# Performance work log

Hardware: AMD Instinct MI355X
Metric: run time of the kernel (lower is better)

The kernel has to match this reference:

```python
import jax, jax.numpy as jnp
import numpy as np

B, S, D_IN, RANK, D_OUT = 8, 1024, 1280, 64, 1280
DOWN_SIZE = RANK * D_IN      # 81920
UP_SIZE = D_OUT * RANK       # 81920


def setup_inputs() -> dict:
    key = jax.random.key(0)
    k1, k2 = jax.random.split(key)
    x = jax.random.normal(k1, (B, S, D_IN), dtype=jnp.float32)
    # per-image embedding that encodes the dynamic LoRA weights
    embed = jax.random.normal(k2, (B, DOWN_SIZE + UP_SIZE), dtype=jnp.float32) * 0.02
    return {"x": x, "embed": embed}


def reference(x, embed):
    # down_forward: per-sample weight = embed[:, :down_size].view(down_shape)=[rank, d_in]
    # original does x_chunk @ W.T per sample; batched as a single grouped GEMM
    w_down = embed[:, :DOWN_SIZE].reshape(B, RANK, D_IN)   # [B, r, d_in]
    h = jnp.einsum('bsd,brd->bsr', x, w_down)              # x @ W_down.T, batched
    # up_forward: per-sample weight = embed[:, -up_size:].view(up_shape)=[d_out, rank]
    w_up = embed[:, -UP_SIZE:].reshape(B, D_OUT, RANK)     # [B, d_out, r]
    out = jnp.einsum('bsr,bor->bso', h, w_up)              # h @ W_up.T, batched
    return out
```

## Files before the change

### kernel.cpp

```cpp
#include <hip/hip_runtime.h>

#define NB   8
#define S_   1024
#define DIN  1280
#define RANK 64
#define DOUT 1280
#define DOWN (RANK * DIN)
#define EMB  (DOWN + DOUT * RANK)
#define XSTRIDE 1288

typedef __bf16 bf16x8 __attribute__((ext_vector_type(8)));
typedef __bf16 bf16x4 __attribute__((ext_vector_type(4)));
typedef float  f32x4  __attribute__((ext_vector_type(4)));

__global__ __launch_bounds__(256) void cvt_embed(const float* __restrict__ src,
                                                 __bf16* __restrict__ dst, int n8) {
    const int i = blockIdx.x * 256 + threadIdx.x;
    if (i < n8) {
        const float4* s = reinterpret_cast<const float4*>(src) + (size_t)i * 2;
        float4 f0 = s[0], f1 = s[1];
        bf16x8 v;
        v[0]=(__bf16)f0.x; v[1]=(__bf16)f0.y; v[2]=(__bf16)f0.z; v[3]=(__bf16)f0.w;
        v[4]=(__bf16)f1.x; v[5]=(__bf16)f1.y; v[6]=(__bf16)f1.z; v[7]=(__bf16)f1.w;
        *reinterpret_cast<bf16x8*>(dst + (size_t)i * 8) = v;
    }
}

__global__ __launch_bounds__(512, 2) void lora_main(const float* __restrict__ x,
                                                    const __bf16* __restrict__ ew,
                                                    float* __restrict__ out) {
    __shared__ __bf16 xls[16 * XSTRIDE];
    __shared__ float  pbuf[4][16][20];
    __shared__ __bf16 hld[16][80];

    const int b    = blockIdx.x & 7;
    const int s0   = (blockIdx.x >> 3) * 16;
    const int t    = threadIdx.x;
    const int w    = t >> 6;
    const int l    = t & 63;
    const int quad = l >> 4;
    const int lc   = l & 15;
    const int dq   = quad * 8;

    {
        const int row = t >> 5;
        const int c   = t & 31;
        const float4* src = reinterpret_cast<const float4*>(x + (size_t)(b * S_ + s0 + row) * DIN);
        __bf16* drow = xls + row * XSTRIDE;
#pragma unroll
        for (int j = 0; j < 10; ++j) {
            float4 f = src[c + 32 * j];
            bf16x4 v;
            v[0]=(__bf16)f.x; v[1]=(__bf16)f.y; v[2]=(__bf16)f.z; v[3]=(__bf16)f.w;
            *reinterpret_cast<bf16x4*>(drow + c * 4 + 128 * j) = v;
        }
    }
    __syncthreads();

    const int nt = w & 3;
    const int kh = w >> 2;
    const __bf16* wdrow  = ew + (size_t)b * EMB + (size_t)(nt * 16 + lc) * DIN + kh * 640;
    const __bf16* xlsrow = xls + lc * XSTRIDE + kh * 640;

    f32x4 acc = {0,0,0,0};
#pragma unroll 5
    for (int ks = 0; ks < 20; ++ks) {
        const int k = ks * 32 + dq;
        bf16x8 af = *reinterpret_cast<const bf16x8*>(xlsrow + k);
        bf16x8 bf = *reinterpret_cast<const bf16x8*>(wdrow + k);
        acc = __builtin_amdgcn_mfma_f32_16x16x32_bf16(af, bf, acc, 0, 0, 0);
    }

    if (kh == 1) {
#pragma unroll
        for (int i = 0; i < 4; ++i) pbuf[nt][quad * 4 + i][lc] = acc[i];
    }
    __syncthreads();
    if (kh == 0) {
#pragma unroll
        for (int i = 0; i < 4; ++i) {
            float v = acc[i] + pbuf[nt][quad * 4 + i][lc];
            hld[quad * 4 + i][nt * 16 + lc] = (__bf16)v;
        }
    }
    __syncthreads();

    bf16x8 ha0 = *reinterpret_cast<const bf16x8*>(&hld[lc][dq]);
    bf16x8 ha1 = *reinterpret_cast<const bf16x8*>(&hld[lc][32 + dq]);
    const __bf16* wu    = ew + (size_t)b * EMB + DOWN;
    float*        obase = out + (size_t)(b * S_ + s0 + quad * 4) * DOUT;

#pragma unroll 2
    for (int tt = 0; tt < 10; ++tt) {
        const int n = w + 8 * tt;
        const int o = n * 16 + lc;
        bf16x8 b0 = *reinterpret_cast<const bf16x8*>(wu + (size_t)o * RANK + dq);
        bf16x8 b1 = *reinterpret_cast<const bf16x8*>(wu + (size_t)o * RANK + 32 + dq);
        f32x4 c = {0,0,0,0};
        c = __builtin_amdgcn_mfma_f32_16x16x32_bf16(ha0, b0, c, 0, 0, 0);
        c = __builtin_amdgcn_mfma_f32_16x16x32_bf16(ha1, b1, c, 0, 0, 0);
#pragma unroll
        for (int i = 0; i < 4; ++i)
            obase[(size_t)i * DOUT + o] = c[i];
    }
}

extern "C" void kernel_launch(void* const* d_in, const int* in_sizes, int n_in,
                              void* d_out, int out_size, void* d_ws, size_t ws_size,
                              hipStream_t stream) {
    const float* x     = (const float*)d_in[0];
    const float* embed = (const float*)d_in[1];
    float*       out   = (float*)d_out;
    __bf16*      ew    = (__bf16*)d_ws;
    (void)in_sizes; (void)n_in; (void)out_size; (void)ws_size;

    cvt_embed<<<dim3(640), dim3(256), 0, stream>>>(embed, ew, NB * EMB / 8);
    lora_main<<<dim3(512), dim3(512), 0, stream>>>(x, ew, out);
}
```

Before: 109.3 us.

## Split fused LoRA kernel into separate down and up kernels with split-K partials

Splits the fused LoRA kernel into two. The down projection runs as 1024 smaller blocks, each handling half of the K dimension and writing fp32 partial h values to workspace. The up projection kernel sums the two partials, converts them to bf16 and does the second GEMM. This aims to raise parallelism and occupancy and shrink the shared-memory footprint, at the cost of an extra launch and a global round trip for the partial h values.

```diff
diff --git a/kernel.cpp b/kernel.cpp
--- a/kernel.cpp
+++ b/kernel.cpp
@@ -7,11 +7,20 @@
 #define DOUT 1280
 #define DOWN (RANK * DIN)
 #define EMB  (DOWN + DOUT * RANK)
-#define XSTRIDE 1288
+#define XSTR 648
 
 typedef __bf16 bf16x8 __attribute__((ext_vector_type(8)));
 typedef __bf16 bf16x4 __attribute__((ext_vector_type(4)));
 typedef float  f32x4  __attribute__((ext_vector_type(4)));
+
+#define PH_OFF (NB * EMB)
+
+__device__ __forceinline__ bf16x8 cvt8(float4 a, float4 b) {
+    bf16x8 r;
+    r[0] = (__bf16)a.x; r[1] = (__bf16)a.y; r[2] = (__bf16)a.z; r[3] = (__bf16)a.w;
+    r[4] = (__bf16)b.x; r[5] = (__bf16)b.y; r[6] = (__bf16)b.z; r[7] = (__bf16)b.w;
+    return r;
+}
 
 __global__ __launch_bounds__(256) void cvt_embed(const float* __restrict__ src,
                                                  __bf16* __restrict__ dst, int n8) {
@@ -19,22 +28,19 @@
     if (i < n8) {
         const float4* s = reinterpret_cast<const float4*>(src) + (size_t)i * 2;
         float4 f0 = s[0], f1 = s[1];
-        bf16x8 v;
-        v[0]=(__bf16)f0.x; v[1]=(__bf16)f0.y; v[2]=(__bf16)f0.z; v[3]=(__bf16)f0.w;
-        v[4]=(__bf16)f1.x; v[5]=(__bf16)f1.y; v[6]=(__bf16)f1.z; v[7]=(__bf16)f1.w;
-        *reinterpret_cast<bf16x8*>(dst + (size_t)i * 8) = v;
+        *reinterpret_cast<bf16x8*>(dst + (size_t)i * 8) = cvt8(f0, f1);
     }
 }
 
-__global__ __launch_bounds__(512, 2) void lora_main(const float* __restrict__ x,
+__global__ __launch_bounds__(256, 4) void lora_down(const float* __restrict__ x,
                                                     const __bf16* __restrict__ ew,
-                                                    float* __restrict__ out) {
-    __shared__ __bf16 xls[16 * XSTRIDE];
-    __shared__ float  pbuf[4][16][20];
-    __shared__ __bf16 hld[16][80];
+                                                    float* __restrict__ ph) {
+    __shared__ __bf16 xls[16 * XSTR];
 
-    const int b    = blockIdx.x & 7;
-    const int s0   = (blockIdx.x >> 3) * 16;
+    const int bid  = blockIdx.x;
+    const int b    = bid & 7;
+    const int st   = (bid >> 3) & 63;
+    const int kh   = bid >> 9;
     const int t    = threadIdx.x;
     const int w    = t >> 6;
     const int l    = t & 63;
@@ -43,62 +49,83 @@
     const int dq   = quad * 8;
 
     {
-        const int row = t >> 5;
-        const int c   = t & 31;
-        const float4* src = reinterpret_cast<const float4*>(x + (size_t)(b * S_ + s0 + row) * DIN);
-        __bf16* drow = xls + row * XSTRIDE;
+        const int row = t >> 4;
+        const int c   = t & 15;
+        const float4* src = reinterpret_cast<const float4*>(
+            x + (size_t)(b * S_ + st * 16 + row) * DIN + kh * 640);
+        __bf16* drow = xls + row * XSTR;
 #pragma unroll
         for (int j = 0; j < 10; ++j) {
-            float4 f = src[c + 32 * j];
+            float4 f = src[c + 16 * j];
             bf16x4 v;
             v[0]=(__bf16)f.x; v[1]=(__bf16)f.y; v[2]=(__bf16)f.z; v[3]=(__bf16)f.w;
-            *reinterpret_cast<bf16x4*>(drow + c * 4 + 128 * j) = v;
+            *reinterpret_cast<bf16x4*>(drow + (c + 16 * j) * 4) = v;
         }
     }
     __syncthreads();
 
-    const int nt = w & 3;
-    const int kh = w >> 2;
-    const __bf16* wdrow  = ew + (size_t)b * EMB + (size_t)(nt * 16 + lc) * DIN + kh * 640;
-    const __bf16* xlsrow = xls + lc * XSTRIDE + kh * 640;
+    const __bf16* wdrow = ew + (size_t)b * EMB + (size_t)(w * 16 + lc) * DIN + kh * 640;
+    const __bf16* xrow  = xls + lc * XSTR;
 
     f32x4 acc = {0,0,0,0};
-#pragma unroll 5
+#pragma unroll 10
     for (int ks = 0; ks < 20; ++ks) {
         const int k = ks * 32 + dq;
-        bf16x8 af = *reinterpret_cast<const bf16x8*>(xlsrow + k);
+        bf16x8 af = *reinterpret_cast<const bf16x8*>(xrow + k);
         bf16x8 bf = *reinterpret_cast<const bf16x8*>(wdrow + k);
         acc = __builtin_amdgcn_mfma_f32_16x16x32_bf16(af, bf, acc, 0, 0, 0);
     }
 
-    if (kh == 1) {
+    float* pdst = ph + ((((size_t)kh * NB + b) * 64 + st) * 16) * 64;
 #pragma unroll
-        for (int i = 0; i < 4; ++i) pbuf[nt][quad * 4 + i][lc] = acc[i];
+    for (int i = 0; i < 4; ++i)
+        pdst[(size_t)(quad * 4 + i) * 64 + w * 16 + lc] = acc[i];
+}
+
+__global__ __launch_bounds__(512, 4) void lora_up(const float* __restrict__ ph,
+                                                  const __bf16* __restrict__ ew,
+                                                  float* __restrict__ out) {
+    const int bid  = blockIdx.x;
+    const int b    = bid & 7;
+    const int st   = bid >> 3;
+    const int w    = threadIdx.x >> 6;
+    const int l    = threadIdx.x & 63;
+    const int quad = l >> 4;
+    const int lc   = l & 15;
+    const int dq   = quad * 8;
+
+    const float* p0 = ph + (((size_t)b * 64 + st) * 16 + lc) * 64;
+    const float* p1 = p0 + (size_t)NB * 64 * 16 * 64;
+    f32x4 a00 = *reinterpret_cast<const f32x4*>(p0 + dq);
+    f32x4 a01 = *reinterpret_cast<const f32x4*>(p0 + dq + 4);
+    f32x4 a10 = *reinterpret_cast<const f32x4*>(p0 + 32 + dq);
+    f32x4 a11 = *reinterpret_cast<const f32x4*>(p0 + 32 + dq + 4);
+    f32x4 b00 = *reinterpret_cast<const f32x4*>(p1 + dq);
+    f32x4 b01 = *reinterpret_cast<const f32x4*>(p1 + dq + 4);
+    f32x4 b10 = *reinterpret_cast<const f32x4*>(p1 + 32 + dq);
+    f32x4 b11 = *reinterpret_cast<const f32x4*>(p1 + 32 + dq + 4);
+    f32x4 s0 = a00 + b00, s1 = a01 + b01, s2 = a10 + b10, s3 = a11 + b11;
+    bf16x8 ha0, ha1;
+#pragma unroll
+    for (int j = 0; j < 4; ++j) {
+        ha0[j]     = (__bf16)s0[j];
+        ha0[4 + j] = (__bf16)s1[j];
+        ha1[j]     = (__bf16)s2[j];
+        ha1[4 + j] = (__bf16)s3[j];
     }
-    __syncthreads();
-    if (kh == 0) {
-#pragma unroll
-        for (int i = 0; i < 4; ++i) {
-            float v = acc[i] + pbuf[nt][quad * 4 + i][lc];
-            hld[quad * 4 + i][nt * 16 + lc] = (__bf16)v;
-        }
-    }
-    __syncthreads();
 
-    bf16x8 ha0 = *reinterpret_cast<const bf16x8*>(&hld[lc][dq]);
-    bf16x8 ha1 = *reinterpret_cast<const bf16x8*>(&hld[lc][32 + dq]);
     const __bf16* wu    = ew + (size_t)b * EMB + DOWN;
-    float*        obase = out + (size_t)(b * S_ + s0 + quad * 4) * DOUT;
+    float*        obase = out + (size_t)(b * S_ + st * 16 + quad * 4) * DOUT;
 
 #pragma unroll 2
     for (int tt = 0; tt < 10; ++tt) {
         const int n = w + 8 * tt;
         const int o = n * 16 + lc;
-        bf16x8 b0 = *reinterpret_cast<const bf16x8*>(wu + (size_t)o * RANK + dq);
-        bf16x8 b1 = *reinterpret_cast<const bf16x8*>(wu + (size_t)o * RANK + 32 + dq);
+        bf16x8 w0 = *reinterpret_cast<const bf16x8*>(wu + (size_t)o * RANK + dq);
+        bf16x8 w1 = *reinterpret_cast<const bf16x8*>(wu + (size_t)o * RANK + 32 + dq);
         f32x4 c = {0,0,0,0};
-        c = __builtin_amdgcn_mfma_f32_16x16x32_bf16(ha0, b0, c, 0, 0, 0);
-        c = __builtin_amdgcn_mfma_f32_16x16x32_bf16(ha1, b1, c, 0, 0, 0);
+        c = __builtin_amdgcn_mfma_f32_16x16x32_bf16(ha0, w0, c, 0, 0, 0);
+        c = __builtin_amdgcn_mfma_f32_16x16x32_bf16(ha1, w1, c, 0, 0, 0);
 #pragma unroll
         for (int i = 0; i < 4; ++i)
             obase[(size_t)i * DOUT + o] = c[i];
@@ -112,8 +139,10 @@
     const float* embed = (const float*)d_in[1];
     float*       out   = (float*)d_out;
     __bf16*      ew    = (__bf16*)d_ws;
+    float*       ph    = (float*)((char*)d_ws + (size_t)NB * EMB * 2);
     (void)in_sizes; (void)n_in; (void)out_size; (void)ws_size;
 
     cvt_embed<<<dim3(640), dim3(256), 0, stream>>>(embed, ew, NB * EMB / 8);
-    lora_main<<<dim3(512), dim3(512), 0, stream>>>(x, ew, out);
+    lora_down<<<dim3(1024), dim3(256), 0, stream>>>(x, ew, ph);
+    lora_up<<<dim3(512), dim3(512), 0, stream>>>(ph, ew, out);
 }
```

Result: slower. 115.1 us (+5.2%).

## Stage up-projection output through LDS for coalesced float4 stores and prefetch weights

Applied to the files above, without the earlier changes.

The up-projection results are now written into a shared-memory buffer that reuses the x staging area. They are then stored to global memory as contiguous float4 rows in 256-column chunks, replacing scattered 4-byte stores. The first eight down-projection weight fragments are loaded before the x staging, and the next chunk's up-projection weights are fetched while the current chunk is written out. The launch-bounds occupancy hint rises to 4 blocks per CU; this adds more barriers per block and may increase register pressure.

```diff
diff --git a/kernel.cpp b/kernel.cpp
--- a/kernel.cpp
+++ b/kernel.cpp
@@ -7,11 +7,19 @@
 #define DOUT 1280
 #define DOWN (RANK * DIN)
 #define EMB  (DOWN + DOUT * RANK)
-#define XSTRIDE 1288
+#define XSTR 1288
+#define OSTR 268
 
 typedef __bf16 bf16x8 __attribute__((ext_vector_type(8)));
 typedef __bf16 bf16x4 __attribute__((ext_vector_type(4)));
 typedef float  f32x4  __attribute__((ext_vector_type(4)));
+
+__device__ __forceinline__ bf16x8 cvt8(float4 a, float4 b) {
+    bf16x8 r;
+    r[0] = (__bf16)a.x; r[1] = (__bf16)a.y; r[2] = (__bf16)a.z; r[3] = (__bf16)a.w;
+    r[4] = (__bf16)b.x; r[5] = (__bf16)b.y; r[6] = (__bf16)b.z; r[7] = (__bf16)b.w;
+    return r;
+}
 
 __global__ __launch_bounds__(256) void cvt_embed(const float* __restrict__ src,
                                                  __bf16* __restrict__ dst, int n8) {
@@ -19,17 +27,17 @@
     if (i < n8) {
         const float4* s = reinterpret_cast<const float4*>(src) + (size_t)i * 2;
         float4 f0 = s[0], f1 = s[1];
-        bf16x8 v;
-        v[0]=(__bf16)f0.x; v[1]=(__bf16)f0.y; v[2]=(__bf16)f0.z; v[3]=(__bf16)f0.w;
-        v[4]=(__bf16)f1.x; v[5]=(__bf16)f1.y; v[6]=(__bf16)f1.z; v[7]=(__bf16)f1.w;
-        *reinterpret_cast<bf16x8*>(dst + (size_t)i * 8) = v;
+        *reinterpret_cast<bf16x8*>(dst + (size_t)i * 8) = cvt8(f0, f1);
     }
 }
 
-__global__ __launch_bounds__(512, 2) void lora_main(const float* __restrict__ x,
+__global__ __launch_bounds__(512, 4) void lora_main(const float* __restrict__ x,
                                                     const __bf16* __restrict__ ew,
                                                     float* __restrict__ out) {
-    __shared__ __bf16 xls[16 * XSTRIDE];
+    __shared__ union {
+        __bf16 xls[16 * XSTR];
+        float  obuf[16 * OSTR];
+    } u;
     __shared__ float  pbuf[4][16][20];
     __shared__ __bf16 hld[16][80];
 
@@ -42,31 +50,51 @@
     const int lc   = l & 15;
     const int dq   = quad * 8;
 
+    const int nt = w & 3;
+    const int kh = w >> 2;
+    const __bf16* wdrow = ew + (size_t)b * EMB + (size_t)(nt * 16 + lc) * DIN + kh * 640;
+
+    bf16x8 pf0 = *reinterpret_cast<const bf16x8*>(wdrow + 0 * 32 + dq);
+    bf16x8 pf1 = *reinterpret_cast<const bf16x8*>(wdrow + 1 * 32 + dq);
+    bf16x8 pf2 = *reinterpret_cast<const bf16x8*>(wdrow + 2 * 32 + dq);
+    bf16x8 pf3 = *reinterpret_cast<const bf16x8*>(wdrow + 3 * 32 + dq);
+    bf16x8 pf4 = *reinterpret_cast<const bf16x8*>(wdrow + 4 * 32 + dq);
+    bf16x8 pf5 = *reinterpret_cast<const bf16x8*>(wdrow + 5 * 32 + dq);
+    bf16x8 pf6 = *reinterpret_cast<const bf16x8*>(wdrow + 6 * 32 + dq);
+    bf16x8 pf7 = *reinterpret_cast<const bf16x8*>(wdrow + 7 * 32 + dq);
+
     {
         const int row = t >> 5;
         const int c   = t & 31;
         const float4* src = reinterpret_cast<const float4*>(x + (size_t)(b * S_ + s0 + row) * DIN);
-        __bf16* drow = xls + row * XSTRIDE;
+        __bf16* drow = u.xls + row * XSTR;
 #pragma unroll
         for (int j = 0; j < 10; ++j) {
             float4 f = src[c + 32 * j];
             bf16x4 v;
             v[0]=(__bf16)f.x; v[1]=(__bf16)f.y; v[2]=(__bf16)f.z; v[3]=(__bf16)f.w;
-            *reinterpret_cast<bf16x4*>(drow + c * 4 + 128 * j) = v;
+            *reinterpret_cast<bf16x4*>(drow + (c + 32 * j) * 4) = v;
         }
     }
     __syncthreads();
 
-    const int nt = w & 3;
-    const int kh = w >> 2;
-    const __bf16* wdrow  = ew + (size_t)b * EMB + (size_t)(nt * 16 + lc) * DIN + kh * 640;
-    const __bf16* xlsrow = xls + lc * XSTRIDE + kh * 640;
-
+    const __bf16* xrow = u.xls + lc * XSTR + kh * 640;
     f32x4 acc = {0,0,0,0};
-#pragma unroll 5
-    for (int ks = 0; ks < 20; ++ks) {
+    {
+        bf16x8 af;
+        af = *reinterpret_cast<const bf16x8*>(xrow + 0*32 + dq); acc = __builtin_amdgcn_mfma_f32_16x16x32_bf16(af, pf0, acc, 0,0,0);
+        af = *reinterpret_cast<const bf16x8*>(xrow + 1*32 + dq); acc = __builtin_amdgcn_mfma_f32_16x16x32_bf16(af, pf1, acc, 0,0,0);
+        af = *reinterpret_cast<const bf16x8*>(xrow + 2*32 + dq); acc = __builtin_amdgcn_mfma_f32_16x16x32_bf16(af, pf2, acc, 0,0,0);
+        af = *reinterpret_cast<const bf16x8*>(xrow + 3*32 + dq); acc = __builtin_amdgcn_mfma_f32_16x16x32_bf16(af, pf3, acc, 0,0,0);
+        af = *reinterpret_cast<const bf16x8*>(xrow + 4*32 + dq); acc = __builtin_amdgcn_mfma_f32_16x16x32_bf16(af, pf4, acc, 0,0,0);
+        af = *reinterpret_cast<const bf16x8*>(xrow + 5*32 + dq); acc = __builtin_amdgcn_mfma_f32_16x16x32_bf16(af, pf5, acc, 0,0,0);
+        af = *reinterpret_cast<const bf16x8*>(xrow + 6*32 + dq); acc = __builtin_amdgcn_mfma_f32_16x16x32_bf16(af, pf6, acc, 0,0,0);
+        af = *reinterpret_cast<const bf16x8*>(xrow + 7*32 + dq); acc = __builtin_amdgcn_mfma_f32_16x16x32_bf16(af, pf7, acc, 0,0,0);
+    }
+#pragma unroll
+    for (int ks = 8; ks < 20; ++ks) {
         const int k = ks * 32 + dq;
-        bf16x8 af = *reinterpret_cast<const bf16x8*>(xlsrow + k);
+        bf16x8 af = *reinterpret_cast<const bf16x8*>(xrow + k);
         bf16x8 bf = *reinterpret_cast<const bf16x8*>(wdrow + k);
         acc = __builtin_amdgcn_mfma_f32_16x16x32_bf16(af, bf, acc, 0, 0, 0);
     }
@@ -87,21 +115,55 @@
 
     bf16x8 ha0 = *reinterpret_cast<const bf16x8*>(&hld[lc][dq]);
     bf16x8 ha1 = *reinterpret_cast<const bf16x8*>(&hld[lc][32 + dq]);
-    const __bf16* wu    = ew + (size_t)b * EMB + DOWN;
-    float*        obase = out + (size_t)(b * S_ + s0 + quad * 4) * DOUT;
+    const __bf16* wu = ew + (size_t)b * EMB + DOWN;
+    float* orow_base = out + (size_t)(b * S_ + s0) * DOUT;
 
-#pragma unroll 2
-    for (int tt = 0; tt < 10; ++tt) {
-        const int n = w + 8 * tt;
-        const int o = n * 16 + lc;
-        bf16x8 b0 = *reinterpret_cast<const bf16x8*>(wu + (size_t)o * RANK + dq);
-        bf16x8 b1 = *reinterpret_cast<const bf16x8*>(wu + (size_t)o * RANK + 32 + dq);
-        f32x4 c = {0,0,0,0};
-        c = __builtin_amdgcn_mfma_f32_16x16x32_bf16(ha0, b0, c, 0, 0, 0);
-        c = __builtin_amdgcn_mfma_f32_16x16x32_bf16(ha1, b1, c, 0, 0, 0);
+    const int frow = t >> 5;
+    const int fc   = t & 31;
+
+    bf16x8 w00, w01, w10, w11;
+    {
+        const int o0 = (w * 2 + 0) * 16 + lc;
+        const int o1 = (w * 2 + 1) * 16 + lc;
+        w00 = *reinterpret_cast<const bf16x8*>(wu + (size_t)o0 * RANK + dq);
+        w01 = *reinterpret_cast<const bf16x8*>(wu + (size_t)o0 * RANK + 32 + dq);
+        w10 = *reinterpret_cast<const bf16x8*>(wu + (size_t)o1 * RANK + dq);
+        w11 = *reinterpret_cast<const bf16x8*>(wu + (size_t)o1 * RANK + 32 + dq);
+    }
+
 #pragma unroll
-        for (int i = 0; i < 4; ++i)
-            obase[(size_t)i * DOUT + o] = c[i];
+    for (int chunk = 0; chunk < 5; ++chunk) {
+        if (chunk) __syncthreads();
+
+        f32x4 c0 = {0,0,0,0}, c1 = {0,0,0,0};
+        c0 = __builtin_amdgcn_mfma_f32_16x16x32_bf16(ha0, w00, c0, 0, 0, 0);
+        c0 = __builtin_amdgcn_mfma_f32_16x16x32_bf16(ha1, w01, c0, 0, 0, 0);
+        c1 = __builtin_amdgcn_mfma_f32_16x16x32_bf16(ha0, w10, c1, 0, 0, 0);
+        c1 = __builtin_amdgcn_mfma_f32_16x16x32_bf16(ha1, w11, c1, 0, 0, 0);
+
+        const int nl0 = w * 2, nl1 = w * 2 + 1;
+#pragma unroll
+        for (int i = 0; i < 4; ++i) {
+            u.obuf[(quad * 4 + i) * OSTR + nl0 * 16 + lc] = c0[i];
+            u.obuf[(quad * 4 + i) * OSTR + nl1 * 16 + lc] = c1[i];
+        }
+
+        if (chunk < 4) {
+            const int o0 = ((chunk + 1) * 16 + w * 2 + 0) * 16 + lc;
+            const int o1 = ((chunk + 1) * 16 + w * 2 + 1) * 16 + lc;
+            w00 = *reinterpret_cast<const bf16x8*>(wu + (size_t)o0 * RANK + dq);
+            w01 = *reinterpret_cast<const bf16x8*>(wu + (size_t)o0 * RANK + 32 + dq);
+            w10 = *reinterpret_cast<const bf16x8*>(wu + (size_t)o1 * RANK + dq);
+            w11 = *reinterpret_cast<const bf16x8*>(wu + (size_t)o1 * RANK + 32 + dq);
+        }
+        __syncthreads();
+
+        const float* orow = u.obuf + frow * OSTR;
+        float4 v0 = *reinterpret_cast<const float4*>(orow + fc * 4);
+        float4 v1 = *reinterpret_cast<const float4*>(orow + (fc + 32) * 4);
+        float* dst = orow_base + (size_t)frow * DOUT + chunk * 256;
+        *reinterpret_cast<float4*>(dst + fc * 4) = v0;
+        *reinterpret_cast<float4*>(dst + (fc + 32) * 4) = v1;
     }
 }
 
```

New measurement: 109.9 us. No clear change (+0.5%).
